# Performance work log

Measured on AMD Instinct MI355X. Metric: run time of the kernel, lower is better.

The kernel has to match this reference:

```python
import jax, jax.numpy as jnp
import numpy as np

N, E, IN, HID, H, OUT = 10000, 160000, 256, 64, 8, 16
NEG_SLOPE = 0.2  # PyG GATConv leaky_relu slope


def _layer_norm(x, g, b, eps=1e-5):
    m = x.mean(-1, keepdims=True)
    v = ((x - m) ** 2).mean(-1, keepdims=True)
    return (x - m) * jax.lax.rsqrt(v + eps) * g + b


def _gat_conv(x, src, dst, W, a_src, a_dst, bias, concat):
    # PyG GATConv: h = x @ W -> [N,H,C]; e_ij = leakyrelu(a_src.h_j + a_dst.h_i);
    # alpha = segment-softmax over incoming edges at dst; out_i = sum_j alpha_ij h_j
    n = x.shape[0]
    heads, c = a_src.shape
    h = (x @ W).reshape(n, heads, c)
    al_s = (h * a_src[None]).sum(-1)  # [N,H]
    al_d = (h * a_dst[None]).sum(-1)  # [N,H]
    e = al_s[src] + al_d[dst]         # [Etot,H]
    e = jnp.where(e > 0, e, NEG_SLOPE * e)
    m = jax.ops.segment_max(e, dst, num_segments=n)
    p = jnp.exp(e - m[dst])
    s = jax.ops.segment_sum(p, dst, num_segments=n)
    a = p / (s[dst] + 1e-16)          # [Etot,H]
    out = jax.ops.segment_sum(h[src] * a[:, :, None], dst, num_segments=n)
    out = out.reshape(n, heads * c) if concat else out.mean(axis=1)
    return out + bias


def setup_inputs() -> dict:
    key = jax.random.key(0)
    ks = jax.random.split(key, 12)
    d = {}
    d['x'] = jax.random.normal(ks[0], (N, IN), jnp.float32)
    d['edge_index'] = jax.random.randint(ks[1], (2, E), 0, N, jnp.int64)
    d['Wp'] = jax.random.normal(ks[2], (IN, HID * H), jnp.float32) * 0.05
    d['bp'] = jnp.zeros((HID * H,), jnp.float32)
    d['g0'] = jnp.ones((HID * H,), jnp.float32)
    d['b0'] = jnp.zeros((HID * H,), jnp.float32)
    d['W1'] = jax.random.normal(ks[3], (HID * H, HID * H), jnp.float32) * 0.05
    d['as1'] = jax.random.normal(ks[4], (H, HID), jnp.float32) * 0.1
    d['ad1'] = jax.random.normal(ks[5], (H, HID), jnp.float32) * 0.1
    d['b1'] = jnp.zeros((HID * H,), jnp.float32)
    d['g1'] = jnp.ones((HID * H,), jnp.float32)
    d['be1'] = jnp.zeros((HID * H,), jnp.float32)
    d['W2'] = jax.random.normal(ks[6], (HID * H, HID * H), jnp.float32) * 0.05
    d['as2'] = jax.random.normal(ks[7], (H, HID), jnp.float32) * 0.1
    d['ad2'] = jax.random.normal(ks[8], (H, HID), jnp.float32) * 0.1
    d['b2'] = jnp.zeros((HID * H,), jnp.float32)
    d['g2'] = jnp.ones((HID * H,), jnp.float32)
    d['be2'] = jnp.zeros((HID * H,), jnp.float32)
    d['W3'] = jax.random.normal(ks[9], (HID * H, OUT), jnp.float32) * 0.05
    d['as3'] = jax.random.normal(ks[10], (1, OUT), jnp.float32) * 0.1
    d['ad3'] = jax.random.normal(ks[11], (1, OUT), jnp.float32) * 0.1
    d['b3'] = jnp.zeros((OUT,), jnp.float32)
    d['g3'] = jnp.ones((OUT,), jnp.float32)
    d['be3'] = jnp.zeros((OUT,), jnp.float32)
    return d


def reference(x, edge_index, Wp, bp, g0, b0, W1, as1, ad1, b1, g1, be1,
              W2, as2, ad2, b2, g2, be2, W3, as3, ad3, b3, g3, be3):
    n = x.shape[0]
    loops = jnp.arange(n)  # PyG add_self_loops=True
    src = jnp.concatenate([edge_index[0], loops])
    dst = jnp.concatenate([edge_index[1], loops])
    x = jax.nn.elu(_layer_norm(x @ Wp + bp, g0, b0))
    # layer 1 (heads=8, concat) + residual
    r = x
    x = _gat_conv(x, src, dst, W1, as1, ad1, b1, True)
    x = jax.nn.elu(_layer_norm(x, g1, be1)) + r
    # layer 2 (heads=8, concat) + residual
    r = x
    x = _gat_conv(x, src, dst, W2, as2, ad2, b2, True)
    x = jax.nn.elu(_layer_norm(x, g2, be2)) + r
    # final layer (heads=1, mean/no-concat), no elu/residual
    x = _gat_conv(x, src, dst, W3, as3, ad3, b3, False)
    x = _layer_norm(x, g3, be3)
    return x
```

## Files before the change

kernel.cpp:

```cpp
#include <hip/hip_runtime.h>
#include <hip/hip_bf16.h>

#define NNODES 10000
#define NEDGES 160000
#define ETOT   (NEDGES + NNODES)
#define CIN    256
#define CH     512
#define NHEAD  8
#define HDIM   64
#define COUT   16
#define NEG_SLOPE 0.2f
#define NF ((size_t)NNODES * CH)

__device__ __forceinline__ float bf2f(uint u) {
    union { uint i; float f; } v; v.i = u << 16; return v.f;
}
__device__ __forceinline__ ushort f2bf(float x) {
    union { float f; uint i; } v; v.f = x;
    uint r = v.i + 0x7fff + ((v.i >> 16) & 1);
    return (ushort)(r >> 16);
}

typedef __attribute__((ext_vector_type(8))) short short8v;
typedef __attribute__((ext_vector_type(4))) float f32x4;

__global__ void count_deg_k(const int* __restrict__ ei, int* __restrict__ deg) {
    int eid = blockIdx.x * 256 + threadIdx.x;
    if (eid >= ETOT) return;
    int dst = (eid < NEDGES) ? ei[NEDGES + eid] : (eid - NEDGES);
    atomicAdd(&deg[dst], 1);
}

__global__ __launch_bounds__(512) void scan_k(const int* __restrict__ deg, int* __restrict__ startA) {
    __shared__ int partial[512];
    int t = threadIdx.x;
    const int per = (NNODES + 511) / 512;
    int base = t * per;
    int s = 0;
    for (int j = 0; j < per; ++j) { int idx = base + j; if (idx < NNODES) s += deg[idx]; }
    partial[t] = s;
    __syncthreads();
    for (int off = 1; off < 512; off <<= 1) {
        int v = (t >= off) ? partial[t - off] : 0;
        __syncthreads();
        partial[t] += v;
        __syncthreads();
    }
    int run = (t == 0) ? 0 : partial[t - 1];
    for (int j = 0; j < per; ++j) {
        int idx = base + j;
        if (idx < NNODES) { startA[idx] = run; run += deg[idx]; }
    }
}

__global__ void scatter_k(const int* __restrict__ ei, const int* __restrict__ startA,
                          int* __restrict__ cursor, int* __restrict__ csr_src) {
    int eid = blockIdx.x * 256 + threadIdx.x;
    if (eid >= ETOT) return;
    int src, dst;
    if (eid < NEDGES) { src = ei[eid]; dst = ei[NEDGES + eid]; }
    else { src = dst = eid - NEDGES; }
    int pos = startA[dst] + atomicAdd(&cursor[dst], 1);
    csr_src[pos] = src;
}

__global__ void convert_x_k(const float* __restrict__ x, ushort* __restrict__ xb) {
    int idx = blockIdx.x * 256 + threadIdx.x;
    if (idx >= NNODES * CIN / 4) return;
    float4 v = ((const float4*)x)[idx];
    ushort4 o; o.x = f2bf(v.x); o.y = f2bf(v.y); o.z = f2bf(v.z); o.w = f2bf(v.w);
    ((ushort4*)xb)[idx] = o;
}

__global__ __launch_bounds__(256) void convert_wT_k(const float* __restrict__ W, ushort* __restrict__ Wt,
                                                    int K, int N) {
    __shared__ float tile[32][33];
    int tx = threadIdx.x & 31, ty = threadIdx.x >> 5;
    int n0 = blockIdx.x * 32, k0 = blockIdx.y * 32;
#pragma unroll
    for (int r = 0; r < 32; r += 8)
        tile[ty + r][tx] = W[(size_t)(k0 + ty + r) * N + n0 + tx];
    __syncthreads();
#pragma unroll
    for (int r = 0; r < 32; r += 8)
        Wt[(size_t)(n0 + ty + r) * K + k0 + tx] = f2bf(tile[tx][ty + r]);
}

#define LDK 40
__global__ __launch_bounds__(256) void gemm_mfma(const ushort* __restrict__ A, const ushort* __restrict__ Bt,
                                                 const float* __restrict__ bias, ushort* __restrict__ C,
                                                 int M, int K) {
    __shared__ ushort Asl[64 * LDK];
    __shared__ ushort Bsl[64 * LDK];
    int t = threadIdx.x;
    int wid = t >> 6, lane = t & 63;
    int row0 = blockIdx.x * 64, col0 = blockIdx.y * 64;
    int wr = (wid >> 1) * 32, wc = (wid & 1) * 32;
    f32x4 acc[2][2] = {};
    int sRow = t >> 2;
    int sK = (t & 3) * 8;
    int lr = lane & 15;
    int kg = (lane >> 4) * 8;

    for (int k0 = 0; k0 < K; k0 += 32) {
        int gr = row0 + sRow;
        uint4 av = {0u, 0u, 0u, 0u};
        if (gr < M) av = *(const uint4*)(A + (size_t)gr * K + k0 + sK);
        *(uint4*)(&Asl[sRow * LDK + sK]) = av;
        uint4 bv = *(const uint4*)(Bt + (size_t)(col0 + sRow) * K + k0 + sK);
        *(uint4*)(&Bsl[sRow * LDK + sK]) = bv;
        __syncthreads();
        short8v a0 = *(const short8v*)(&Asl[(wr + lr) * LDK + kg]);
        short8v a1 = *(const short8v*)(&Asl[(wr + 16 + lr) * LDK + kg]);
        short8v b0 = *(const short8v*)(&Bsl[(wc + lr) * LDK + kg]);
        short8v b1 = *(const short8v*)(&Bsl[(wc + 16 + lr) * LDK + kg]);
        acc[0][0] = __builtin_amdgcn_mfma_f32_16x16x32_bf16(a0, b0, acc[0][0], 0, 0, 0);
        acc[0][1] = __builtin_amdgcn_mfma_f32_16x16x32_bf16(a0, b1, acc[0][1], 0, 0, 0);
        acc[1][0] = __builtin_amdgcn_mfma_f32_16x16x32_bf16(a1, b0, acc[1][0], 0, 0, 0);
        acc[1][1] = __builtin_amdgcn_mfma_f32_16x16x32_bf16(a1, b1, acc[1][1], 0, 0, 0);
        __syncthreads();
    }
#pragma unroll
    for (int mf = 0; mf < 2; ++mf) {
#pragma unroll
        for (int nf = 0; nf < 2; ++nf) {
            int c = col0 + wc + nf * 16 + lr;
            float bb = bias ? bias[c] : 0.f;
#pragma unroll
            for (int j = 0; j < 4; ++j) {
                int r = row0 + wr + mf * 16 + (lane >> 4) * 4 + j;
                if (r < M) C[(size_t)r * CH + c] = f2bf(acc[mf][nf][j] + bb);
            }
        }
    }
}

__global__ __launch_bounds__(128) void ln_elu_k(const ushort* __restrict__ inb, const float* __restrict__ g,
                                                const float* __restrict__ b, ushort* __restrict__ outb) {
    int i = blockIdx.x, t = threadIdx.x;
    uint2 hv = ((const uint2*)(inb + (size_t)i * CH))[t];
    float a0 = bf2f(hv.x & 0xffff), a1 = bf2f(hv.x >> 16);
    float a2 = bf2f(hv.y & 0xffff), a3 = bf2f(hv.y >> 16);
    float s = a0 + a1 + a2 + a3;
    float s2 = a0 * a0 + a1 * a1 + a2 * a2 + a3 * a3;
#pragma unroll
    for (int off = 1; off < 64; off <<= 1) { s += __shfl_xor(s, off); s2 += __shfl_xor(s2, off); }
    __shared__ float sh[4];
    int wid = t >> 6, lane = t & 63;
    if (lane == 0) { sh[wid] = s; sh[2 + wid] = s2; }
    __syncthreads();
    float tot = sh[0] + sh[1], tot2 = sh[2] + sh[3];
    float mean = tot * (1.0f / CH);
    float var = tot2 * (1.0f / CH) - mean * mean;
    float rstd = rsqrtf(var + 1e-5f);
    float4 gv = ((const float4*)g)[t];
    float4 bv = ((const float4*)b)[t];
    float y0 = (a0 - mean) * rstd * gv.x + bv.x; y0 = y0 > 0.f ? y0 : __expf(y0) - 1.f;
    float y1 = (a1 - mean) * rstd * gv.y + bv.y; y1 = y1 > 0.f ? y1 : __expf(y1) - 1.f;
    float y2 = (a2 - mean) * rstd * gv.z + bv.z; y2 = y2 > 0.f ? y2 : __expf(y2) - 1.f;
    float y3 = (a3 - mean) * rstd * gv.w + bv.w; y3 = y3 > 0.f ? y3 : __expf(y3) - 1.f;
    ushort4 o; o.x = f2bf(y0); o.y = f2bf(y1); o.z = f2bf(y2); o.w = f2bf(y3);
    ((ushort4*)(outb + (size_t)i * CH))[t] = o;
}

__global__ void attn_logits_k(const ushort* __restrict__ h, const float* __restrict__ a_src,
                              const float* __restrict__ a_dst, float* __restrict__ als,
                              float* __restrict__ ald) {
    int idx = blockIdx.x * 256 + threadIdx.x;
    if (idx >= NNODES * NHEAD) return;
    int i = idx >> 3, hh = idx & 7;
    const uint2* hp = (const uint2*)(h + (size_t)i * CH + hh * HDIM);
    const float* sp = a_src + hh * HDIM;
    const float* dp = a_dst + hh * HDIM;
    float s = 0.f, d = 0.f;
#pragma unroll
    for (int j = 0; j < HDIM / 4; ++j) {
        uint2 v = hp[j];
        float h0 = bf2f(v.x & 0xffff), h1 = bf2f(v.x >> 16);
        float h2 = bf2f(v.y & 0xffff), h3 = bf2f(v.y >> 16);
        s += h0 * sp[j * 4] + h1 * sp[j * 4 + 1] + h2 * sp[j * 4 + 2] + h3 * sp[j * 4 + 3];
        d += h0 * dp[j * 4] + h1 * dp[j * 4 + 1] + h2 * dp[j * 4 + 2] + h3 * dp[j * 4 + 3];
    }
    als[idx] = s; ald[idx] = d;
}

__global__ __launch_bounds__(128) void agg_ln_k(const ushort* __restrict__ hb, const float* __restrict__ als,
                                                const float* __restrict__ ald, const int* __restrict__ startA,
                                                const int* __restrict__ deg, const int* __restrict__ csr,
                                                const float* __restrict__ bias, const float* __restrict__ gamma,
                                                const float* __restrict__ beta, const ushort* __restrict__ residb,
                                                ushort* __restrict__ outb) {
    int i = blockIdx.x, t = threadIdx.x;
    int c0 = t * 4, head = t >> 4;
    int s0 = startA[i], d = deg[i];
    float aldv = ald[i * NHEAD + head];
    const int* cp = csr + s0;
    float m = -1e30f;
    for (int e = 0; e < d; ++e) {
        int src = cp[e];
        float ee = als[src * NHEAD + head] + aldv;
        ee = ee > 0.f ? ee : NEG_SLOPE * ee;
        m = fmaxf(m, ee);
    }
    float ssum = 0.f;
    float a0 = 0.f, a1 = 0.f, a2 = 0.f, a3 = 0.f;
    for (int e = 0; e < d; ++e) {
        int src = cp[e];
        float ee = als[src * NHEAD + head] + aldv;
        ee = ee > 0.f ? ee : NEG_SLOPE * ee;
        float p = __expf(ee - m);
        ssum += p;
        uint2 hv = *(const uint2*)(hb + (size_t)src * CH + c0);
        a0 += p * bf2f(hv.x & 0xffff); a1 += p * bf2f(hv.x >> 16);
        a2 += p * bf2f(hv.y & 0xffff); a3 += p * bf2f(hv.y >> 16);
    }
    float inv = 1.0f / (ssum + 1e-16f);
    float4 bi = ((const float4*)bias)[t];
    a0 = a0 * inv + bi.x; a1 = a1 * inv + bi.y; a2 = a2 * inv + bi.z; a3 = a3 * inv + bi.w;
    float s = a0 + a1 + a2 + a3;
    float s2 = a0 * a0 + a1 * a1 + a2 * a2 + a3 * a3;
#pragma unroll
    for (int off = 1; off < 64; off <<= 1) { s += __shfl_xor(s, off); s2 += __shfl_xor(s2, off); }
    __shared__ float sh[4];
    int wid = t >> 6, lane = t & 63;
    if (lane == 0) { sh[wid] = s; sh[2 + wid] = s2; }
    __syncthreads();
    float tot = sh[0] + sh[1], tot2 = sh[2] + sh[3];
    float mean = tot * (1.0f / CH);
    float var = tot2 * (1.0f / CH) - mean * mean;
    float rstd = rsqrtf(var + 1e-5f);
    float4 gv = ((const float4*)gamma)[t];
    float4 bv = ((const float4*)beta)[t];
    uint2 rv = ((const uint2*)(residb + (size_t)i * CH))[t];
    float y0 = (a0 - mean) * rstd * gv.x + bv.x; y0 = (y0 > 0.f ? y0 : __expf(y0) - 1.f) + bf2f(rv.x & 0xffff);
    float y1 = (a1 - mean) * rstd * gv.y + bv.y; y1 = (y1 > 0.f ? y1 : __expf(y1) - 1.f) + bf2f(rv.x >> 16);
    float y2 = (a2 - mean) * rstd * gv.z + bv.z; y2 = (y2 > 0.f ? y2 : __expf(y2) - 1.f) + bf2f(rv.y & 0xffff);
    float y3 = (a3 - mean) * rstd * gv.w + bv.w; y3 = (y3 > 0.f ? y3 : __expf(y3) - 1.f) + bf2f(rv.y >> 16);
    ushort4 o; o.x = f2bf(y0); o.y = f2bf(y1); o.z = f2bf(y2); o.w = f2bf(y3);
    ((ushort4*)(outb + (size_t)i * CH))[t] = o;
}

__global__ __launch_bounds__(256) void gemm_small_k(const ushort* __restrict__ A, const float* __restrict__ W,
                                                    float* __restrict__ C) {
    int col = threadIdx.x & 15;
    int row = blockIdx.x * 16 + (threadIdx.x >> 4);
    if (row >= NNODES) return;
    const ushort* ar = A + (size_t)row * CH;
    float acc = 0.f;
#pragma unroll 8
    for (int k = 0; k < CH; k += 2) {
        uint av = *(const uint*)(ar + k);
        acc += bf2f(av & 0xffff) * W[k * COUT + col];
        acc += bf2f(av >> 16) * W[(k + 1) * COUT + col];
    }
    C[row * COUT + col] = acc;
}

__global__ __launch_bounds__(256) void agg16f_k(const float* __restrict__ h3, const float* __restrict__ as3,
                                                const float* __restrict__ ad3, const int* __restrict__ startA,
                                                const int* __restrict__ deg, const int* __restrict__ csr,
                                                const float* __restrict__ b3, const float* __restrict__ g3,
                                                const float* __restrict__ be3, float* __restrict__ out) {
    int t = threadIdx.x;
    int i = blockIdx.x * 16 + (t >> 4);
    int c = t & 15;
    if (i >= NNODES) return;
    float asc = as3[c], adc = ad3[c];
    float ald_i = h3[i * COUT + c] * adc;
#pragma unroll
    for (int off = 1; off < 16; off <<= 1) ald_i += __shfl_xor(ald_i, off, 16);
    int s0 = startA[i], d = deg[i];
    float m = -1e30f;
    for (int e = 0; e < d; ++e) {
        int src = csr[s0 + e];
        float al = h3[src * COUT + c] * asc;
#pragma unroll
        for (int off = 1; off < 16; off <<= 1) al += __shfl_xor(al, off, 16);
        float ee = al + ald_i;
        ee = ee > 0.f ? ee : NEG_SLOPE * ee;
        m = fmaxf(m, ee);
    }
    float ssum = 0.f, acc = 0.f;
    for (int e = 0; e < d; ++e) {
        int src = csr[s0 + e];
        float v = h3[src * COUT + c];
        float al = v * asc;
#pragma unroll
        for (int off = 1; off < 16; off <<= 1) al += __shfl_xor(al, off, 16);
        float ee = al + ald_i;
        ee = ee > 0.f ? ee : NEG_SLOPE * ee;
        float p = __expf(ee - m);
        ssum += p;
        acc += p * v;
    }
    acc = acc / (ssum + 1e-16f) + b3[c];
    float v = acc, v2 = acc * acc;
#pragma unroll
    for (int off = 1; off < 16; off <<= 1) { v += __shfl_xor(v, off, 16); v2 += __shfl_xor(v2, off, 16); }
    float mean = v * (1.0f / COUT);
    float var = v2 * (1.0f / COUT) - mean * mean;
    out[i * COUT + c] = (acc - mean) * rsqrtf(var + 1e-5f) * g3[c] + be3[c];
}

extern "C" void kernel_launch(void* const* d_in, const int* in_sizes, int n_in,
                              void* d_out, int out_size, void* d_ws, size_t ws_size,
                              hipStream_t stream) {
    const float* x   = (const float*)d_in[0];
    const int*   ei  = (const int*)d_in[1];
    const float* Wp  = (const float*)d_in[2];
    const float* bp  = (const float*)d_in[3];
    const float* g0  = (const float*)d_in[4];
    const float* b0  = (const float*)d_in[5];
    const float* W1  = (const float*)d_in[6];
    const float* as1 = (const float*)d_in[7];
    const float* ad1 = (const float*)d_in[8];
    const float* b1  = (const float*)d_in[9];
    const float* g1  = (const float*)d_in[10];
    const float* be1 = (const float*)d_in[11];
    const float* W2  = (const float*)d_in[12];
    const float* as2 = (const float*)d_in[13];
    const float* ad2 = (const float*)d_in[14];
    const float* b2  = (const float*)d_in[15];
    const float* g2  = (const float*)d_in[16];
    const float* be2 = (const float*)d_in[17];
    const float* W3  = (const float*)d_in[18];
    const float* as3 = (const float*)d_in[19];
    const float* ad3 = (const float*)d_in[20];
    const float* b3  = (const float*)d_in[21];
    const float* g3  = (const float*)d_in[22];
    const float* be3 = (const float*)d_in[23];

    ushort* B0  = (ushort*)d_ws;
    ushort* B1  = B0 + NF;
    ushort* B2  = B1 + NF;
    ushort* xbf = B2 + NF;
    ushort* Wpt = xbf + (size_t)NNODES * CIN;
    ushort* W1t = Wpt + (size_t)CIN * CH;
    ushort* W2t = W1t + (size_t)CH * CH;
    float* als = (float*)(W2t + (size_t)CH * CH);
    float* ald = als + NNODES * NHEAD;
    float* h3  = ald + NNODES * NHEAD;
    int* deg = (int*)(h3 + (size_t)NNODES * COUT);
    int* stA = deg + NNODES;
    int* cur = stA + NNODES;
    int* csr = cur + NNODES;

    hipMemsetAsync(deg, 0, NNODES * sizeof(int), stream);
    hipMemsetAsync(cur, 0, NNODES * sizeof(int), stream);
    count_deg_k<<<(ETOT + 255) / 256, 256, 0, stream>>>(ei, deg);
    scan_k<<<1, 512, 0, stream>>>(deg, stA);
    scatter_k<<<(ETOT + 255) / 256, 256, 0, stream>>>(ei, stA, cur, csr);

    convert_x_k<<<(NNODES * CIN / 4 + 255) / 256, 256, 0, stream>>>(x, xbf);
    convert_wT_k<<<dim3(CH / 32, CIN / 32), 256, 0, stream>>>(Wp, Wpt, CIN, CH);
    convert_wT_k<<<dim3(CH / 32, CH / 32), 256, 0, stream>>>(W1, W1t, CH, CH);
    convert_wT_k<<<dim3(CH / 32, CH / 32), 256, 0, stream>>>(W2, W2t, CH, CH);

    dim3 gg((NNODES + 63) / 64, CH / 64);

    gemm_mfma<<<gg, 256, 0, stream>>>(xbf, Wpt, bp, B0, NNODES, CIN);
    ln_elu_k<<<NNODES, 128, 0, stream>>>(B0, g0, b0, B1);

    gemm_mfma<<<gg, 256, 0, stream>>>(B1, W1t, nullptr, B2, NNODES, CH);
    attn_logits_k<<<(NNODES * NHEAD + 255) / 256, 256, 0, stream>>>(B2, as1, ad1, als, ald);
    agg_ln_k<<<NNODES, 128, 0, stream>>>(B2, als, ald, stA, deg, csr, b1, g1, be1, B1, B0);

    gemm_mfma<<<gg, 256, 0, stream>>>(B0, W2t, nullptr, B1, NNODES, CH);
    attn_logits_k<<<(NNODES * NHEAD + 255) / 256, 256, 0, stream>>>(B1, as2, ad2, als, ald);
    agg_ln_k<<<NNODES, 128, 0, stream>>>(B1, als, ald, stA, deg, csr, b2, g2, be2, B0, B2);

    gemm_small_k<<<(NNODES + 15) / 16, 256, 0, stream>>>(B2, W3, h3);
    agg16f_k<<<(NNODES + 15) / 16, 256, 0, stream>>>(h3, as3, ad3, stA, deg, csr, b3, g3, be3, (float*)d_out);
}
```

Before: 367.9 us.

## Fuse attention logits into GEMM epilogue and process two nodes per aggregation block

The attention-logit dot products are now computed in the MFMA GEMM epilogue: each 64-column block maps to one head, and partial sums are reduced with shuffles and shared memory. This removes the separate attn_logits kernel and its re-read of h. The GEMM K-step is doubled to 64, giving fewer barriers per tile at the cost of more LDS. The aggregation kernel now handles one node per wavefront with 8 channels per lane via 16-byte loads, which drops the cross-wave LDS reduction and barrier. The cost is more registers per lane and fewer lanes sharing each edge's softmax work.

```diff
diff --git a/kernel.cpp b/kernel.cpp
--- a/kernel.cpp
+++ b/kernel.cpp
@@ -86,50 +86,100 @@
         Wt[(size_t)(n0 + ty + r) * K + k0 + tx] = f2bf(tile[tx][ty + r]);
 }
 
-#define LDK 40
+#define LDB 72
 __global__ __launch_bounds__(256) void gemm_mfma(const ushort* __restrict__ A, const ushort* __restrict__ Bt,
                                                  const float* __restrict__ bias, ushort* __restrict__ C,
+                                                 const float* __restrict__ a_src, const float* __restrict__ a_dst,
+                                                 float* __restrict__ als, float* __restrict__ ald,
                                                  int M, int K) {
-    __shared__ ushort Asl[64 * LDK];
-    __shared__ ushort Bsl[64 * LDK];
+    __shared__ ushort Asl[64 * LDB];
+    __shared__ ushort Bsl[64 * LDB];
+    __shared__ float lals[2][64], lald[2][64];
     int t = threadIdx.x;
     int wid = t >> 6, lane = t & 63;
     int row0 = blockIdx.x * 64, col0 = blockIdx.y * 64;
     int wr = (wid >> 1) * 32, wc = (wid & 1) * 32;
     f32x4 acc[2][2] = {};
     int sRow = t >> 2;
-    int sK = (t & 3) * 8;
+    int sK = (t & 3) * 16;
     int lr = lane & 15;
-    int kg = (lane >> 4) * 8;
-
-    for (int k0 = 0; k0 < K; k0 += 32) {
+    int kg = lane >> 4;
+
+    for (int k0 = 0; k0 < K; k0 += 64) {
         int gr = row0 + sRow;
-        uint4 av = {0u, 0u, 0u, 0u};
-        if (gr < M) av = *(const uint4*)(A + (size_t)gr * K + k0 + sK);
-        *(uint4*)(&Asl[sRow * LDK + sK]) = av;
-        uint4 bv = *(const uint4*)(Bt + (size_t)(col0 + sRow) * K + k0 + sK);
-        *(uint4*)(&Bsl[sRow * LDK + sK]) = bv;
+        uint4 av0 = {0u,0u,0u,0u}, av1 = {0u,0u,0u,0u};
+        if (gr < M) {
+            const ushort* ap = A + (size_t)gr * K + k0 + sK;
+            av0 = *(const uint4*)ap; av1 = *(const uint4*)(ap + 8);
+        }
+        *(uint4*)(&Asl[sRow * LDB + sK]) = av0;
+        *(uint4*)(&Asl[sRow * LDB + sK + 8]) = av1;
+        const ushort* bp = Bt + (size_t)(col0 + sRow) * K + k0 + sK;
+        *(uint4*)(&Bsl[sRow * LDB + sK]) = *(const uint4*)bp;
+        *(uint4*)(&Bsl[sRow * LDB + sK + 8]) = *(const uint4*)(bp + 8);
         __syncthreads();
-        short8v a0 = *(const short8v*)(&Asl[(wr + lr) * LDK + kg]);
-        short8v a1 = *(const short8v*)(&Asl[(wr + 16 + lr) * LDK + kg]);
-        short8v b0 = *(const short8v*)(&Bsl[(wc + lr) * LDK + kg]);
-        short8v b1 = *(const short8v*)(&Bsl[(wc + 16 + lr) * LDK + kg]);
-        acc[0][0] = __builtin_amdgcn_mfma_f32_16x16x32_bf16(a0, b0, acc[0][0], 0, 0, 0);
-        acc[0][1] = __builtin_amdgcn_mfma_f32_16x16x32_bf16(a0, b1, acc[0][1], 0, 0, 0);
-        acc[1][0] = __builtin_amdgcn_mfma_f32_16x16x32_bf16(a1, b0, acc[1][0], 0, 0, 0);
-        acc[1][1] = __builtin_amdgcn_mfma_f32_16x16x32_bf16(a1, b1, acc[1][1], 0, 0, 0);
+#pragma unroll
+        for (int ks = 0; ks < 2; ++ks) {
+            short8v a0 = *(const short8v*)&Asl[(wr + lr) * LDB + ks * 32 + kg * 8];
+            short8v a1 = *(const short8v*)&Asl[(wr + 16 + lr) * LDB + ks * 32 + kg * 8];
+            short8v b0 = *(const short8v*)&Bsl[(wc + lr) * LDB + ks * 32 + kg * 8];
+            short8v b1 = *(const short8v*)&Bsl[(wc + 16 + lr) * LDB + ks * 32 + kg * 8];
+            acc[0][0] = __builtin_amdgcn_mfma_f32_16x16x32_bf16(a0, b0, acc[0][0], 0, 0, 0);
+            acc[0][1] = __builtin_amdgcn_mfma_f32_16x16x32_bf16(a0, b1, acc[0][1], 0, 0, 0);
+            acc[1][0] = __builtin_amdgcn_mfma_f32_16x16x32_bf16(a1, b0, acc[1][0], 0, 0, 0);
+            acc[1][1] = __builtin_amdgcn_mfma_f32_16x16x32_bf16(a1, b1, acc[1][1], 0, 0, 0);
+        }
         __syncthreads();
     }
-#pragma unroll
-    for (int mf = 0; mf < 2; ++mf) {
-#pragma unroll
-        for (int nf = 0; nf < 2; ++nf) {
-            int c = col0 + wc + nf * 16 + lr;
+    float pals[2][4] = {}, pald[2][4] = {};
+    bool doLog = (a_src != nullptr);
+    int head = blockIdx.y;
+#pragma unroll
+    for (int i = 0; i < 2; ++i) {
+#pragma unroll
+        for (int j = 0; j < 2; ++j) {
+            int cl = wc + j * 16 + lr;
+            int c = col0 + cl;
             float bb = bias ? bias[c] : 0.f;
-#pragma unroll
-            for (int j = 0; j < 4; ++j) {
-                int r = row0 + wr + mf * 16 + (lane >> 4) * 4 + j;
-                if (r < M) C[(size_t)r * CH + c] = f2bf(acc[mf][nf][j] + bb);
+            float as_c = doLog ? a_src[head * HDIM + cl] : 0.f;
+            float ad_c = doLog ? a_dst[head * HDIM + cl] : 0.f;
+#pragma unroll
+            for (int q = 0; q < 4; ++q) {
+                int r = row0 + wr + i * 16 + kg * 4 + q;
+                float hv = acc[i][j][q] + bb;
+                if (r < M) C[(size_t)r * CH + c] = f2bf(hv);
+                pals[i][q] += hv * as_c;
+                pald[i][q] += hv * ad_c;
+            }
+        }
+    }
+    if (doLog) {
+#pragma unroll
+        for (int i = 0; i < 2; ++i)
+#pragma unroll
+            for (int q = 0; q < 4; ++q) {
+#pragma unroll
+                for (int off = 1; off < 16; off <<= 1) {
+                    pals[i][q] += __shfl_xor(pals[i][q], off);
+                    pald[i][q] += __shfl_xor(pald[i][q], off);
+                }
+            }
+        if (lr == 0) {
+#pragma unroll
+            for (int i = 0; i < 2; ++i)
+#pragma unroll
+                for (int q = 0; q < 4; ++q) {
+                    int r = wr + i * 16 + kg * 4 + q;
+                    lals[wid & 1][r] = pals[i][q];
+                    lald[wid & 1][r] = pald[i][q];
+                }
+        }
+        __syncthreads();
+        if (t < 64) {
+            int r = row0 + t;
+            if (r < M) {
+                als[r * NHEAD + head] = lals[0][t] + lals[1][t];
+                ald[r * NHEAD + head] = lald[0][t] + lald[1][t];
             }
         }
     }
@@ -163,35 +213,16 @@
     ((ushort4*)(outb + (size_t)i * CH))[t] = o;
 }
 
-__global__ void attn_logits_k(const ushort* __restrict__ h, const float* __restrict__ a_src,
-                              const float* __restrict__ a_dst, float* __restrict__ als,
-                              float* __restrict__ ald) {
-    int idx = blockIdx.x * 256 + threadIdx.x;
-    if (idx >= NNODES * NHEAD) return;
-    int i = idx >> 3, hh = idx & 7;
-    const uint2* hp = (const uint2*)(h + (size_t)i * CH + hh * HDIM);
-    const float* sp = a_src + hh * HDIM;
-    const float* dp = a_dst + hh * HDIM;
-    float s = 0.f, d = 0.f;
-#pragma unroll
-    for (int j = 0; j < HDIM / 4; ++j) {
-        uint2 v = hp[j];
-        float h0 = bf2f(v.x & 0xffff), h1 = bf2f(v.x >> 16);
-        float h2 = bf2f(v.y & 0xffff), h3 = bf2f(v.y >> 16);
-        s += h0 * sp[j * 4] + h1 * sp[j * 4 + 1] + h2 * sp[j * 4 + 2] + h3 * sp[j * 4 + 3];
-        d += h0 * dp[j * 4] + h1 * dp[j * 4 + 1] + h2 * dp[j * 4 + 2] + h3 * dp[j * 4 + 3];
-    }
-    als[idx] = s; ald[idx] = d;
-}
-
 __global__ __launch_bounds__(128) void agg_ln_k(const ushort* __restrict__ hb, const float* __restrict__ als,
                                                 const float* __restrict__ ald, const int* __restrict__ startA,
                                                 const int* __restrict__ deg, const int* __restrict__ csr,
                                                 const float* __restrict__ bias, const float* __restrict__ gamma,
                                                 const float* __restrict__ beta, const ushort* __restrict__ residb,
                                                 ushort* __restrict__ outb) {
-    int i = blockIdx.x, t = threadIdx.x;
-    int c0 = t * 4, head = t >> 4;
+    int t = threadIdx.x;
+    int i = blockIdx.x * 2 + (t >> 6);
+    int tl = t & 63;
+    int c0 = tl * 8, head = tl >> 3;
     int s0 = startA[i], d = deg[i];
     float aldv = ald[i * NHEAD + head];
     const int* cp = csr + s0;
@@ -203,41 +234,47 @@
         m = fmaxf(m, ee);
     }
     float ssum = 0.f;
-    float a0 = 0.f, a1 = 0.f, a2 = 0.f, a3 = 0.f;
+    float a0 = 0, a1 = 0, a2 = 0, a3 = 0, a4 = 0, a5 = 0, a6 = 0, a7 = 0;
     for (int e = 0; e < d; ++e) {
         int src = cp[e];
         float ee = als[src * NHEAD + head] + aldv;
         ee = ee > 0.f ? ee : NEG_SLOPE * ee;
         float p = __expf(ee - m);
         ssum += p;
-        uint2 hv = *(const uint2*)(hb + (size_t)src * CH + c0);
+        uint4 hv = *(const uint4*)(hb + (size_t)src * CH + c0);
         a0 += p * bf2f(hv.x & 0xffff); a1 += p * bf2f(hv.x >> 16);
         a2 += p * bf2f(hv.y & 0xffff); a3 += p * bf2f(hv.y >> 16);
+        a4 += p * bf2f(hv.z & 0xffff); a5 += p * bf2f(hv.z >> 16);
+        a6 += p * bf2f(hv.w & 0xffff); a7 += p * bf2f(hv.w >> 16);
     }
     float inv = 1.0f / (ssum + 1e-16f);
-    float4 bi = ((const float4*)bias)[t];
-    a0 = a0 * inv + bi.x; a1 = a1 * inv + bi.y; a2 = a2 * inv + bi.z; a3 = a3 * inv + bi.w;
-    float s = a0 + a1 + a2 + a3;
-    float s2 = a0 * a0 + a1 * a1 + a2 * a2 + a3 * a3;
+    float4 bi0 = ((const float4*)bias)[tl * 2], bi1 = ((const float4*)bias)[tl * 2 + 1];
+    a0 = a0 * inv + bi0.x; a1 = a1 * inv + bi0.y; a2 = a2 * inv + bi0.z; a3 = a3 * inv + bi0.w;
+    a4 = a4 * inv + bi1.x; a5 = a5 * inv + bi1.y; a6 = a6 * inv + bi1.z; a7 = a7 * inv + bi1.w;
+    float s = a0 + a1 + a2 + a3 + a4 + a5 + a6 + a7;
+    float s2 = a0*a0 + a1*a1 + a2*a2 + a3*a3 + a4*a4 + a5*a5 + a6*a6 + a7*a7;
 #pragma unroll
     for (int off = 1; off < 64; off <<= 1) { s += __shfl_xor(s, off); s2 += __shfl_xor(s2, off); }
-    __shared__ float sh[4];
-    int wid = t >> 6, lane = t & 63;
-    if (lane == 0) { sh[wid] = s; sh[2 + wid] = s2; }
-    __syncthreads();
-    float tot = sh[0] + sh[1], tot2 = sh[2] + sh[3];
-    float mean = tot * (1.0f / CH);
-    float var = tot2 * (1.0f / CH) - mean * mean;
+    float mean = s * (1.0f / CH);
+    float var = s2 * (1.0f / CH) - mean * mean;
     float rstd = rsqrtf(var + 1e-5f);
-    float4 gv = ((const float4*)gamma)[t];
-    float4 bv = ((const float4*)beta)[t];
-    uint2 rv = ((const uint2*)(residb + (size_t)i * CH))[t];
-    float y0 = (a0 - mean) * rstd * gv.x + bv.x; y0 = (y0 > 0.f ? y0 : __expf(y0) - 1.f) + bf2f(rv.x & 0xffff);
-    float y1 = (a1 - mean) * rstd * gv.y + bv.y; y1 = (y1 > 0.f ? y1 : __expf(y1) - 1.f) + bf2f(rv.x >> 16);
-    float y2 = (a2 - mean) * rstd * gv.z + bv.z; y2 = (y2 > 0.f ? y2 : __expf(y2) - 1.f) + bf2f(rv.y & 0xffff);
-    float y3 = (a3 - mean) * rstd * gv.w + bv.w; y3 = (y3 > 0.f ? y3 : __expf(y3) - 1.f) + bf2f(rv.y >> 16);
-    ushort4 o; o.x = f2bf(y0); o.y = f2bf(y1); o.z = f2bf(y2); o.w = f2bf(y3);
-    ((ushort4*)(outb + (size_t)i * CH))[t] = o;
+    float4 gv0 = ((const float4*)gamma)[tl * 2], gv1 = ((const float4*)gamma)[tl * 2 + 1];
+    float4 bv0 = ((const float4*)beta)[tl * 2],  bv1 = ((const float4*)beta)[tl * 2 + 1];
+    uint4 rv = ((const uint4*)(residb + (size_t)i * CH))[tl];
+    float y0 = (a0 - mean) * rstd * gv0.x + bv0.x; y0 = (y0 > 0.f ? y0 : __expf(y0) - 1.f) + bf2f(rv.x & 0xffff);
+    float y1 = (a1 - mean) * rstd * gv0.y + bv0.y; y1 = (y1 > 0.f ? y1 : __expf(y1) - 1.f) + bf2f(rv.x >> 16);
+    float y2 = (a2 - mean) * rstd * gv0.z + bv0.z; y2 = (y2 > 0.f ? y2 : __expf(y2) - 1.f) + bf2f(rv.y & 0xffff);
+    float y3 = (a3 - mean) * rstd * gv0.w + bv0.w; y3 = (y3 > 0.f ? y3 : __expf(y3) - 1.f) + bf2f(rv.y >> 16);
+    float y4 = (a4 - mean) * rstd * gv1.x + bv1.x; y4 = (y4 > 0.f ? y4 : __expf(y4) - 1.f) + bf2f(rv.z & 0xffff);
+    float y5 = (a5 - mean) * rstd * gv1.y + bv1.y; y5 = (y5 > 0.f ? y5 : __expf(y5) - 1.f) + bf2f(rv.z >> 16);
+    float y6 = (a6 - mean) * rstd * gv1.z + bv1.z; y6 = (y6 > 0.f ? y6 : __expf(y6) - 1.f) + bf2f(rv.w & 0xffff);
+    float y7 = (a7 - mean) * rstd * gv1.w + bv1.w; y7 = (y7 > 0.f ? y7 : __expf(y7) - 1.f) + bf2f(rv.w >> 16);
+    uint4 o;
+    o.x = (uint)f2bf(y0) | ((uint)f2bf(y1) << 16);
+    o.y = (uint)f2bf(y2) | ((uint)f2bf(y3) << 16);
+    o.z = (uint)f2bf(y4) | ((uint)f2bf(y5) << 16);
+    o.w = (uint)f2bf(y6) | ((uint)f2bf(y7) << 16);
+    ((uint4*)(outb + (size_t)i * CH))[tl] = o;
 }
 
 __global__ __launch_bounds__(256) void gemm_small_k(const ushort* __restrict__ A, const float* __restrict__ W,
@@ -358,16 +395,14 @@
 
     dim3 gg((NNODES + 63) / 64, CH / 64);
 
-    gemm_mfma<<<gg, 256, 0, stream>>>(xbf, Wpt, bp, B0, NNODES, CIN);
+    gemm_mfma<<<gg, 256, 0, stream>>>(xbf, Wpt, bp, B0, nullptr, nullptr, nullptr, nullptr, NNODES, CIN);
     ln_elu_k<<<NNODES, 128, 0, stream>>>(B0, g0, b0, B1);
 
-    gemm_mfma<<<gg, 256, 0, stream>>>(B1, W1t, nullptr, B2, NNODES, CH);
-    attn_logits_k<<<(NNODES * NHEAD + 255) / 256, 256, 0, stream>>>(B2, as1, ad1, als, ald);
-    agg_ln_k<<<NNODES, 128, 0, stream>>>(B2, als, ald, stA, deg, csr, b1, g1, be1, B1, B0);
-
-    gemm_mfma<<<gg, 256, 0, stream>>>(B0, W2t, nullptr, B1, NNODES, CH);
-    attn_logits_k<<<(NNODES * NHEAD + 255) / 256, 256, 0, stream>>>(B1, as2, ad2, als, ald);
-    agg_ln_k<<<NNODES, 128, 0, stream>>>(B1, als, ald, stA, deg, csr, b2, g2, be2, B0, B2);
+    gemm_mfma<<<gg, 256, 0, stream>>>(B1, W1t, nullptr, B2, as1, ad1, als, ald, NNODES, CH);
+    agg_ln_k<<<NNODES / 2, 128, 0, stream>>>(B2, als, ald, stA, deg, csr, b1, g1, be1, B1, B0);
+
+    gemm_mfma<<<gg, 256, 0, stream>>>(B0, W2t, nullptr, B1, as2, ad2, als, ald, NNODES, CH);
+    agg_ln_k<<<NNODES / 2, 128, 0, stream>>>(B1, als, ald, stA, deg, csr, b2, g2, be2, B0, B2);
 
     gemm_small_k<<<(NNODES + 15) / 16, 256, 0, stream>>>(B2, W3, h3);
     agg16f_k<<<(NNODES + 15) / 16, 256, 0, stream>>>(h3, as3, ad3, stA, deg, csr, b3, g3, be3, (float*)d_out);
```

Result: faster. 349.4 us (-5.0%).
